# Performance work log

Hardware: AMD Instinct MI355X
Metric: run time of the kernel (lower is better)

Reference implementation:

```python
import jax, jax.numpy as jnp
import numpy as np

UNITS = 1024
IN_DIM = 1024
BATCH = 4096


def setup_inputs() -> dict:
    key = jax.random.key(0)
    ks = jax.random.split(key, 11)
    C = UNITS + IN_DIM  # concat dim
    glorot = lambda k, shp: jax.random.uniform(k, shp, jnp.float32, -1.0, 1.0) * np.sqrt(6.0 / (shp[0] + shp[1]))
    return {
        "inputs": jax.random.normal(ks[0], (BATCH, IN_DIM), jnp.float32),
        "hidden_state": jax.random.normal(ks[1], (BATCH, UNITS), jnp.float32),
        "cell_state": jax.random.normal(ks[2], (BATCH, UNITS), jnp.float32),
        "W_f": glorot(ks[3], (C, UNITS)), "b_f": jnp.ones((UNITS,), jnp.float32),  # forget bias init = ones
        "W_i": glorot(ks[4], (C, UNITS)), "b_i": jnp.zeros((UNITS,), jnp.float32),
        "W_c": glorot(ks[5], (C, UNITS)), "b_c": jnp.zeros((UNITS,), jnp.float32),
        "W_o": glorot(ks[6], (C, UNITS)), "b_o": jnp.zeros((UNITS,), jnp.float32),
    }


def reference(inputs, hidden_state, cell_state, W_f, b_f, W_i, b_i, W_c, b_c, W_o, b_o):
    # concat order matches original: (hidden_state, inputs)
    x = jnp.concatenate((hidden_state, inputs), axis=1)  # [B, U+D]
    f = jax.nn.sigmoid(x @ W_f + b_f)
    i = jax.nn.sigmoid(x @ W_i + b_i)
    c_cand = jnp.tanh(x @ W_c + b_c)
    new_cell = f * cell_state + i * c_cand
    o = jax.nn.sigmoid(x @ W_o + b_o)
    new_hidden = o * jnp.tanh(new_cell)
    return (new_hidden, new_cell)
```

## Files before the change

kernel.cpp:

```cpp
#include <hip/hip_runtime.h>
#include <hip/hip_bf16.h>

#define BATCH  4096
#define UNITS  1024
#define CDIM   2048
#define NDIM   4096

typedef __attribute__((ext_vector_type(8))) short bf16x8;
typedef __attribute__((ext_vector_type(4))) float f32x4;

__device__ __forceinline__ void gload_lds16(const void* g, void* l) {
    __builtin_amdgcn_global_load_lds(
        (const __attribute__((address_space(1))) unsigned int*)g,
        (__attribute__((address_space(3))) unsigned int*)l, 16, 0, 0);
}

__device__ __forceinline__ float sigm(float x) { return 1.f / (1.f + __expf(-x)); }
__device__ __forceinline__ float tanh_fast(float x) { return 2.f / (1.f + __expf(-2.f * x)) - 1.f; }

__global__ void prep(const float* __restrict__ h, const float* __restrict__ in,
                     const float* __restrict__ Wf, const float* __restrict__ Wi,
                     const float* __restrict__ Wc, const float* __restrict__ Wo,
                     __hip_bfloat16* __restrict__ x, __hip_bfloat16* __restrict__ Wt) {
    __shared__ float tile[32][33];
    int b = blockIdx.x, tid = threadIdx.x;
    if (b < (BATCH * CDIM / 4) / 256) {
        int t = b * 256 + tid;
        int col = (t % (CDIM / 4)) * 4;
        int row = t / (CDIM / 4);
        const float* src = (col < UNITS) ? (h + (size_t)row * UNITS + col)
                                         : (in + (size_t)row * UNITS + (col - UNITS));
        float4 v = *(const float4*)src;
        __hip_bfloat16* dst = x + (size_t)row * CDIM + col;
        dst[0] = __float2bfloat16(v.x); dst[1] = __float2bfloat16(v.y);
        dst[2] = __float2bfloat16(v.z); dst[3] = __float2bfloat16(v.w);
    } else {
        int idx = b - 8192;
        int g = idx >> 11, rest = idx & 2047, ky = rest >> 5, ux = rest & 31;
        const float* W = (g == 0) ? Wf : (g == 1) ? Wi : (g == 2) ? Wc : Wo;
        int u0 = ux * 32, k0 = ky * 32;
        int tx = tid & 31, ty = tid >> 5;
#pragma unroll
        for (int r = 0; r < 4; ++r)
            tile[ty + r * 8][tx] = W[(size_t)(k0 + ty + r * 8) * UNITS + u0 + tx];
        __syncthreads();
#pragma unroll
        for (int r = 0; r < 4; ++r) {
            int u = u0 + ty + r * 8;
            int n = ((u >> 5) << 7) + (((u >> 4) & 1) << 6) + (g << 4) + (u & 15);
            Wt[(size_t)n * CDIM + k0 + tx] = __float2bfloat16(tile[tx][ty + r * 8]);
        }
    }
}

__global__ __launch_bounds__(256) void gemm_lstm(
    const __hip_bfloat16* __restrict__ A,
    const __hip_bfloat16* __restrict__ Bt,
    const float* __restrict__ b_f, const float* __restrict__ b_i,
    const float* __restrict__ b_c, const float* __restrict__ b_o,
    const float* __restrict__ cell,
    float* __restrict__ out)
{
    __shared__ short As[128 * 64];
    __shared__ short Bs[128 * 64];
    const int K = CDIM;
    int m0 = blockIdx.y * 128, n0 = blockIdx.x * 128;
    int tid  = threadIdx.x;
    int w    = tid >> 6, lane = tid & 63;
    int quad = lane >> 4, r16 = lane & 15;
    int wm = (w & 1) * 64, wn = (w >> 1) * 64;

    f32x4 acc[4][4];
#pragma unroll
    for (int i = 0; i < 4; ++i)
#pragma unroll
        for (int j = 0; j < 4; ++j) acc[i][j] = (f32x4){0.f, 0.f, 0.f, 0.f};

    const short* Ag = (const short*)A  + (size_t)m0 * K;
    const short* Bg = (const short*)Bt + (size_t)n0 * K;

    for (int k0 = 0; k0 < K; k0 += 64) {
        __syncthreads();
#pragma unroll
        for (int p = 0; p < 4; ++p) {
            int s   = p * 256 + tid;
            int row = s >> 3;
            int cg  = (s & 7) ^ (row & 7);
            int lofs = (p * 256 + w * 64) * 8;
            gload_lds16(Ag + (size_t)row * K + k0 + cg * 8, As + lofs);
            gload_lds16(Bg + (size_t)row * K + k0 + cg * 8, Bs + lofs);
        }
        asm volatile("s_waitcnt vmcnt(0)" ::: "memory");
        __syncthreads();

#pragma unroll
        for (int ks = 0; ks < 2; ++ks) {
            bf16x8 af[4], bfr[4];
#pragma unroll
            for (int i = 0; i < 4; ++i) {
                int r = wm + i * 16 + r16;
                af[i]  = *(const bf16x8*)&As[r * 64 + (((quad + ks * 4) ^ (r16 & 7)) * 8)];
            }
#pragma unroll
            for (int j = 0; j < 4; ++j) {
                int r = wn + j * 16 + r16;
                bfr[j] = *(const bf16x8*)&Bs[r * 64 + (((quad + ks * 4) ^ (r16 & 7)) * 8)];
            }
#pragma unroll
            for (int i = 0; i < 4; ++i)
#pragma unroll
                for (int j = 0; j < 4; ++j)
                    acc[i][j] = __builtin_amdgcn_mfma_f32_16x16x32_bf16(af[i], bfr[j], acc[i][j], 0, 0, 0);
        }
    }

    int u = blockIdx.x * 32 + (w >> 1) * 16 + r16;
    float bfv = b_f[u], biv = b_i[u], bcv = b_c[u], bov = b_o[u];
    float* out_h = out;
    float* out_c = out + (size_t)BATCH * UNITS;
#pragma unroll
    for (int i = 0; i < 4; ++i) {
#pragma unroll
        for (int rr = 0; rr < 4; ++rr) {
            int m = m0 + wm + i * 16 + quad * 4 + rr;
            float fg = sigm(acc[i][0][rr] + bfv);
            float ig = sigm(acc[i][1][rr] + biv);
            float cc = tanh_fast(acc[i][2][rr] + bcv);
            float og = sigm(acc[i][3][rr] + bov);
            float cold = cell[(size_t)m * UNITS + u];
            float cn = fg * cold + ig * cc;
            out_h[(size_t)m * UNITS + u] = og * tanh_fast(cn);
            out_c[(size_t)m * UNITS + u] = cn;
        }
    }
}

extern "C" void kernel_launch(void* const* d_in, const int* in_sizes, int n_in,
                              void* d_out, int out_size, void* d_ws, size_t ws_size,
                              hipStream_t stream) {
    const float* inputs = (const float*)d_in[0];
    const float* hidden = (const float*)d_in[1];
    const float* cell   = (const float*)d_in[2];
    const float* Wf = (const float*)d_in[3];
    const float* bf_ = (const float*)d_in[4];
    const float* Wi = (const float*)d_in[5];
    const float* bi_ = (const float*)d_in[6];
    const float* Wc = (const float*)d_in[7];
    const float* bc_ = (const float*)d_in[8];
    const float* Wo = (const float*)d_in[9];
    const float* bo_ = (const float*)d_in[10];
    float* out = (float*)d_out;

    char* ws = (char*)d_ws;
    __hip_bfloat16* x  = (__hip_bfloat16*)ws;
    __hip_bfloat16* Wt = (__hip_bfloat16*)(ws + (16u << 20));

    prep<<<dim3(16384), dim3(256), 0, stream>>>(hidden, inputs, Wf, Wi, Wc, Wo, x, Wt);
    gemm_lstm<<<dim3(NDIM / 128, BATCH / 128), dim3(256), 0, stream>>>(
        x, Wt, bf_, bi_, bc_, bo_, cell, out);
}
```

Before: 222.2 us.

## Use 256x256 tiles with double-buffered LDS and XCD-aware block mapping

Grows the GEMM block tile from 128x128 to 256x256 with 512 threads and 8 waves, each wave computing a 64x128 sub-tile. The K step drops to 32, and the LDS buffers are double-buffered so the next tile's global-to-LDS loads are issued before the current tile's MFMAs. Work goes to a 1D grid of 256 blocks, remapped so that blocks landing on the same XCD share A and B panels in L2. The larger tiles cut global traffic per FLOP, but double the accumulator registers and leave only 256 blocks, roughly one wave of work on 256 CUs, which risks lower occupancy and tail imbalance.

```diff
diff --git a/kernel.cpp b/kernel.cpp
--- a/kernel.cpp
+++ b/kernel.cpp
@@ -53,7 +53,7 @@
     }
 }
 
-__global__ __launch_bounds__(256) void gemm_lstm(
+__global__ __launch_bounds__(512, 2) void gemm_lstm(
     const __hip_bfloat16* __restrict__ A,
     const __hip_bfloat16* __restrict__ Bt,
     const float* __restrict__ b_f, const float* __restrict__ b_i,
@@ -61,76 +61,88 @@
     const float* __restrict__ cell,
     float* __restrict__ out)
 {
-    __shared__ short As[128 * 64];
-    __shared__ short Bs[128 * 64];
+    __shared__ short As[2][256 * 32];
+    __shared__ short Bs[2][256 * 32];
     const int K = CDIM;
-    int m0 = blockIdx.y * 128, n0 = blockIdx.x * 128;
+
+    int bid  = blockIdx.x;
+    int xcd  = bid & 7, slot = bid >> 3;
+    int mi   = (xcd & 3) * 4 + (slot & 3);
+    int ni   = (xcd >> 2) * 8 + (slot >> 2);
+    int m0   = mi * 256, n0 = ni * 256;
+
     int tid  = threadIdx.x;
     int w    = tid >> 6, lane = tid & 63;
     int quad = lane >> 4, r16 = lane & 15;
-    int wm = (w & 1) * 64, wn = (w >> 1) * 64;
+    int wm   = (w & 3) * 64;
+    int wc   = w >> 2;
+    int wn   = wc * 128;
 
-    f32x4 acc[4][4];
+    f32x4 acc[4][8];
 #pragma unroll
     for (int i = 0; i < 4; ++i)
 #pragma unroll
-        for (int j = 0; j < 4; ++j) acc[i][j] = (f32x4){0.f, 0.f, 0.f, 0.f};
+        for (int j = 0; j < 8; ++j) acc[i][j] = (f32x4){0.f, 0.f, 0.f, 0.f};
 
     const short* Ag = (const short*)A  + (size_t)m0 * K;
     const short* Bg = (const short*)Bt + (size_t)n0 * K;
 
-    for (int k0 = 0; k0 < K; k0 += 64) {
-        __syncthreads();
+    auto stage = [&](int p, int k0) {
 #pragma unroll
-        for (int p = 0; p < 4; ++p) {
-            int s   = p * 256 + tid;
-            int row = s >> 3;
-            int cg  = (s & 7) ^ (row & 7);
-            int lofs = (p * 256 + w * 64) * 8;
-            gload_lds16(Ag + (size_t)row * K + k0 + cg * 8, As + lofs);
-            gload_lds16(Bg + (size_t)row * K + k0 + cg * 8, Bs + lofs);
+        for (int q = 0; q < 2; ++q) {
+            int s    = q * 512 + tid;
+            int row  = s >> 2;
+            int cg   = (s & 3) ^ (row & 3);
+            int lofs = (q * 512 + w * 64) * 8;
+            gload_lds16(Ag + (size_t)row * K + k0 + cg * 8, &As[p][lofs]);
+            gload_lds16(Bg + (size_t)row * K + k0 + cg * 8, &Bs[p][lofs]);
         }
+    };
+
+    stage(0, 0);
+    int kofs = (quad ^ (r16 & 3)) * 8;
+
+    for (int kt = 0; kt < K / 32; ++kt) {
+        int p = kt & 1;
         asm volatile("s_waitcnt vmcnt(0)" ::: "memory");
         __syncthreads();
+        if (kt + 1 < K / 32) stage(1 - p, (kt + 1) * 32);
 
+        bf16x8 af[4], bb[8];
 #pragma unroll
-        for (int ks = 0; ks < 2; ++ks) {
-            bf16x8 af[4], bfr[4];
+        for (int i = 0; i < 4; ++i)
+            af[i] = *(const bf16x8*)&As[p][(wm + i * 16 + r16) * 32 + kofs];
 #pragma unroll
-            for (int i = 0; i < 4; ++i) {
-                int r = wm + i * 16 + r16;
-                af[i]  = *(const bf16x8*)&As[r * 64 + (((quad + ks * 4) ^ (r16 & 7)) * 8)];
-            }
+        for (int j = 0; j < 8; ++j)
+            bb[j] = *(const bf16x8*)&Bs[p][(wn + j * 16 + r16) * 32 + kofs];
 #pragma unroll
-            for (int j = 0; j < 4; ++j) {
-                int r = wn + j * 16 + r16;
-                bfr[j] = *(const bf16x8*)&Bs[r * 64 + (((quad + ks * 4) ^ (r16 & 7)) * 8)];
-            }
+        for (int i = 0; i < 4; ++i)
 #pragma unroll
-            for (int i = 0; i < 4; ++i)
-#pragma unroll
-                for (int j = 0; j < 4; ++j)
-                    acc[i][j] = __builtin_amdgcn_mfma_f32_16x16x32_bf16(af[i], bfr[j], acc[i][j], 0, 0, 0);
-        }
+            for (int j = 0; j < 8; ++j)
+                acc[i][j] = __builtin_amdgcn_mfma_f32_16x16x32_bf16(af[i], bb[j], acc[i][j], 0, 0, 0);
     }
 
-    int u = blockIdx.x * 32 + (w >> 1) * 16 + r16;
-    float bfv = b_f[u], biv = b_i[u], bcv = b_c[u], bov = b_o[u];
     float* out_h = out;
     float* out_c = out + (size_t)BATCH * UNITS;
+    int ub = ni * 64 + wc * 32 + r16;
 #pragma unroll
-    for (int i = 0; i < 4; ++i) {
+    for (int grp = 0; grp < 2; ++grp) {
+        int u = ub + grp * 16;
+        float bfv = b_f[u], biv = b_i[u], bcv = b_c[u], bov = b_o[u];
 #pragma unroll
-        for (int rr = 0; rr < 4; ++rr) {
-            int m = m0 + wm + i * 16 + quad * 4 + rr;
-            float fg = sigm(acc[i][0][rr] + bfv);
-            float ig = sigm(acc[i][1][rr] + biv);
-            float cc = tanh_fast(acc[i][2][rr] + bcv);
-            float og = sigm(acc[i][3][rr] + bov);
-            float cold = cell[(size_t)m * UNITS + u];
-            float cn = fg * cold + ig * cc;
-            out_h[(size_t)m * UNITS + u] = og * tanh_fast(cn);
-            out_c[(size_t)m * UNITS + u] = cn;
+        for (int i = 0; i < 4; ++i) {
+#pragma unroll
+            for (int rr = 0; rr < 4; ++rr) {
+                int m = m0 + wm + i * 16 + quad * 4 + rr;
+                float fg = sigm(acc[i][grp * 4 + 0][rr] + bfv);
+                float ig = sigm(acc[i][grp * 4 + 1][rr] + biv);
+                float cc = tanh_fast(acc[i][grp * 4 + 2][rr] + bcv);
+                float og = sigm(acc[i][grp * 4 + 3][rr] + bov);
+                float cold = cell[(size_t)m * UNITS + u];
+                float cn = fg * cold + ig * cc;
+                out_h[(size_t)m * UNITS + u] = og * tanh_fast(cn);
+                out_c[(size_t)m * UNITS + u] = cn;
+            }
         }
     }
 }
@@ -156,6 +168,6 @@
     __hip_bfloat16* Wt = (__hip_bfloat16*)(ws + (16u << 20));
 
     prep<<<dim3(16384), dim3(256), 0, stream>>>(hidden, inputs, Wf, Wi, Wc, Wo, x, Wt);
-    gemm_lstm<<<dim3(NDIM / 128, BATCH / 128), dim3(256), 0, stream>>>(
+    gemm_lstm<<<dim3(256), dim3(512), 0, stream>>>(
         x, Wt, bf_, bi_, bc_, bo_, cell, out);
 }
```

Result: slower. 231.7 us (+4.3%).

## Double-buffer A tile in LDS, load B fragments directly to registers, enlarge tile

Applied to the files above, without the earlier changes.

Changes the GEMM tile to 128x256 per block, with each wave owning a 64-wide slice of N. The B fragments are loaded straight from global memory into registers and prefetched one K step ahead. The A tile is double-buffered in LDS so the next stage loads during the MFMA work, and a 1D grid with a swizzled block mapping is used. The aim is to overlap memory with compute and halve syncs per K step, at the cost of much higher register pressure (128 accumulator floats plus 16 B fragments) and uncoalesced direct B loads.

```diff
diff --git a/kernel.cpp b/kernel.cpp
--- a/kernel.cpp
+++ b/kernel.cpp
@@ -53,7 +53,7 @@
     }
 }
 
-__global__ __launch_bounds__(256) void gemm_lstm(
+__global__ __launch_bounds__(256, 2) void gemm_lstm(
     const __hip_bfloat16* __restrict__ A,
     const __hip_bfloat16* __restrict__ Bt,
     const float* __restrict__ b_f, const float* __restrict__ b_i,
@@ -61,68 +61,86 @@
     const float* __restrict__ cell,
     float* __restrict__ out)
 {
-    __shared__ short As[128 * 64];
-    __shared__ short Bs[128 * 64];
+    __shared__ short As[2][128 * 64];
     const int K = CDIM;
-    int m0 = blockIdx.y * 128, n0 = blockIdx.x * 128;
+
+    int bid = blockIdx.x;
+    int nb  = (bid & 7) * 2 + ((bid >> 3) & 1);
+    int mb  = bid >> 4;
+    int m0  = mb * 128, n0 = nb * 256;
+
     int tid  = threadIdx.x;
     int w    = tid >> 6, lane = tid & 63;
     int quad = lane >> 4, r16 = lane & 15;
-    int wm = (w & 1) * 64, wn = (w >> 1) * 64;
+    int wn   = w * 64;
 
-    f32x4 acc[4][4];
+    f32x4 acc[8][4];
 #pragma unroll
-    for (int i = 0; i < 4; ++i)
+    for (int i = 0; i < 8; ++i)
 #pragma unroll
         for (int j = 0; j < 4; ++j) acc[i][j] = (f32x4){0.f, 0.f, 0.f, 0.f};
 
     const short* Ag = (const short*)A  + (size_t)m0 * K;
-    const short* Bg = (const short*)Bt + (size_t)n0 * K;
+    const short* Bg = (const short*)Bt + (size_t)(n0 + wn + r16) * K + quad * 8;
 
-    for (int k0 = 0; k0 < K; k0 += 64) {
-        __syncthreads();
+    auto stageA = [&](int p, int k0) {
 #pragma unroll
-        for (int p = 0; p < 4; ++p) {
-            int s   = p * 256 + tid;
-            int row = s >> 3;
-            int cg  = (s & 7) ^ (row & 7);
-            int lofs = (p * 256 + w * 64) * 8;
-            gload_lds16(Ag + (size_t)row * K + k0 + cg * 8, As + lofs);
-            gload_lds16(Bg + (size_t)row * K + k0 + cg * 8, Bs + lofs);
+        for (int q = 0; q < 4; ++q) {
+            int s    = q * 256 + tid;
+            int row  = s >> 3;
+            int cg   = (s & 7) ^ (row & 7);
+            int lofs = (q * 256 + w * 64) * 8;
+            gload_lds16(Ag + (size_t)row * K + k0 + cg * 8, &As[p][lofs]);
         }
+    };
+
+    bf16x8 bcur[8], bnxt[8];
+#pragma unroll
+    for (int ks = 0; ks < 2; ++ks)
+#pragma unroll
+        for (int j = 0; j < 4; ++j)
+            bcur[ks * 4 + j] = *(const bf16x8*)&Bg[(size_t)(j * 16) * K + ks * 32];
+    stageA(0, 0);
+
+    for (int kt = 0; kt < K / 64; ++kt) {
+        int p = kt & 1;
         asm volatile("s_waitcnt vmcnt(0)" ::: "memory");
         __syncthreads();
-
+        if (kt + 1 < K / 64) {
+            stageA(1 - p, (kt + 1) * 64);
+            int kb = (kt + 1) * 64;
+#pragma unroll
+            for (int ks = 0; ks < 2; ++ks)
+#pragma unroll
+                for (int j = 0; j < 4; ++j)
+                    bnxt[ks * 4 + j] = *(const bf16x8*)&Bg[(size_t)(j * 16) * K + kb + ks * 32];
+        }
 #pragma unroll
         for (int ks = 0; ks < 2; ++ks) {
-            bf16x8 af[4], bfr[4];
+            bf16x8 af[8];
+            int kc = ((quad + ks * 4) ^ (r16 & 7)) * 8;
 #pragma unroll
-            for (int i = 0; i < 4; ++i) {
-                int r = wm + i * 16 + r16;
-                af[i]  = *(const bf16x8*)&As[r * 64 + (((quad + ks * 4) ^ (r16 & 7)) * 8)];
-            }
+            for (int i = 0; i < 8; ++i)
+                af[i] = *(const bf16x8*)&As[p][(i * 16 + r16) * 64 + kc];
 #pragma unroll
-            for (int j = 0; j < 4; ++j) {
-                int r = wn + j * 16 + r16;
-                bfr[j] = *(const bf16x8*)&Bs[r * 64 + (((quad + ks * 4) ^ (r16 & 7)) * 8)];
-            }
-#pragma unroll
-            for (int i = 0; i < 4; ++i)
+            for (int i = 0; i < 8; ++i)
 #pragma unroll
                 for (int j = 0; j < 4; ++j)
-                    acc[i][j] = __builtin_amdgcn_mfma_f32_16x16x32_bf16(af[i], bfr[j], acc[i][j], 0, 0, 0);
+                    acc[i][j] = __builtin_amdgcn_mfma_f32_16x16x32_bf16(af[i], bcur[ks * 4 + j], acc[i][j], 0, 0, 0);
         }
+#pragma unroll
+        for (int t = 0; t < 8; ++t) bcur[t] = bnxt[t];
     }
 
-    int u = blockIdx.x * 32 + (w >> 1) * 16 + r16;
+    int u = nb * 64 + (w >> 1) * 32 + (w & 1) * 16 + r16;
     float bfv = b_f[u], biv = b_i[u], bcv = b_c[u], bov = b_o[u];
     float* out_h = out;
     float* out_c = out + (size_t)BATCH * UNITS;
 #pragma unroll
-    for (int i = 0; i < 4; ++i) {
+    for (int i = 0; i < 8; ++i) {
 #pragma unroll
         for (int rr = 0; rr < 4; ++rr) {
-            int m = m0 + wm + i * 16 + quad * 4 + rr;
+            int m = m0 + i * 16 + quad * 4 + rr;
             float fg = sigm(acc[i][0][rr] + bfv);
             float ig = sigm(acc[i][1][rr] + biv);
             float cc = tanh_fast(acc[i][2][rr] + bcv);
@@ -156,6 +174,6 @@
     __hip_bfloat16* Wt = (__hip_bfloat16*)(ws + (16u << 20));
 
     prep<<<dim3(16384), dim3(256), 0, stream>>>(hidden, inputs, Wf, Wi, Wc, Wo, x, Wt);
-    gemm_lstm<<<dim3(NDIM / 128, BATCH / 128), dim3(256), 0, stream>>>(
+    gemm_lstm<<<dim3(512), dim3(256), 0, stream>>>(
         x, Wt, bf_, bi_, bc_, bo_, cell, out);
 }
```

New measurement: 219.8 us. No clear change (-1.1%).
